# Performance work log

Hardware: AMD Instinct MI355X
Metric: run time of the kernel (lower is better)

The kernel has to match this reference:

```python
import jax, jax.numpy as jnp
import numpy as np

B, C, H, W, Q = 8, 64, 32, 32, 8
K = 2 ** Q  # codebook size = 256


def setup_inputs() -> dict:
    key = jax.random.key(0)
    k0, k1, k2, k3, k4, k5 = jax.random.split(key, 6)
    x = jax.random.normal(k0, (B, C, H, W), dtype=jnp.float32)
    # grouped 1x1 conv C -> Q*C with groups=C: per-channel weight [C, Q]
    w_pre = jax.random.normal(k1, (C, Q), dtype=jnp.float32) * 0.1
    b_pre = jax.random.normal(k2, (C, Q), dtype=jnp.float32) * 0.01
    # codebook init: uniform(-1/2^Q, 1/2^Q) as in nn.Embedding init in the module
    codebook = jax.random.uniform(k3, (K, Q), dtype=jnp.float32, minval=-1.0 / K, maxval=1.0 / K)
    # grouped 1x1 conv Q*C -> C with groups=C: per-channel weight [C, Q]
    w_after = jax.random.normal(k4, (C, Q), dtype=jnp.float32) * 0.1
    b_after = jax.random.normal(k5, (C,), dtype=jnp.float32) * 0.01
    return {"x": x, "w_pre": w_pre, "b_pre": b_pre, "codebook": codebook,
            "w_after": w_after, "b_after": b_after}


def reference(x, w_pre, b_pre, codebook, w_after, b_after):
    sg = jax.lax.stop_gradient
    Bn, Cn, Hn, Wn = x.shape
    Qn = w_pre.shape[1]
    # pre_quant: grouped 1x1 conv (groups=C): each input channel c -> Q outputs
    # y[b,c,q,h,w] = x[b,c,h,w] * w_pre[c,q] + b_pre[c,q]
    y = x[:, :, None, :, :] * w_pre[None, :, :, None, None] + b_pre[None, :, :, None, None]
    # torch permutes [B, C*Q, H, W] -> [B, H, W, C*Q] then reshapes to (-1, Q);
    # out-channel order is c*Q+q, so rows are (b,h,w,c) blocks of Q features.
    xq = jnp.transpose(y, (0, 3, 4, 1, 2))  # [B, H, W, C, Q]
    flat = xq.reshape(-1, Qn)  # [N, Q]
    cb = codebook  # [K, Q]
    # squared euclidean distances [N, K]
    dist = (jnp.sum(flat * flat, axis=1, keepdims=True)
            + jnp.sum(cb * cb, axis=1)
            - 2.0 * flat @ cb.T)
    idx = jnp.argmin(dist, axis=1)  # [N]
    out = cb[idx]  # gather == one-hot @ codebook, same math
    kl_loss = (jnp.mean((sg(out) - flat) ** 2)
               + 0.25 * jnp.mean((out - sg(flat)) ** 2))
    # straight-through
    bit = flat + sg(out - flat)  # [N, Q]
    bit5 = bit.reshape(Bn, Hn, Wn, Cn, Qn)
    bit_cqhw = jnp.transpose(bit5, (0, 3, 4, 1, 2))  # [B, C, Q, H, W]
    bit_out = bit_cqhw.reshape(Bn, Cn * Qn, Hn, Wn)
    # after_quant: grouped 1x1 conv (groups=C): Q inputs per channel -> 1 output
    recon = (jnp.einsum('bcqhw,cq->bchw', bit_cqhw, w_after)
             + b_after[None, :, None, None])
    return kl_loss, bit_out, recon
```

## Files before the change

kernel.cpp:

```cpp
#include <hip/hip_runtime.h>
#include <float.h>

#define NB 8
#define NC 64
#define NH 32
#define NW 32
#define NQ 8
#define NK 256
#define NROWS (NB*NC*NH*NW)
#define TPB 256
#define RPB 1024
#define NBLK2 (NROWS/RPB)
#define BIT_OFF 1
#define REC_OFF (1 + NROWS*NQ)

#define WS_BREAKS(ws) ((double*)(ws))
#define WS_SEGCB(ws)  ((float*)((char*)(ws) + 196608))
#define WS_SEGR(ws)   ((float*)((char*)(ws) + 720896))
#define WS_SEGBG(ws)  ((double*)((char*)(ws) + 786432))
#define WS_ALPHA(ws)  ((double*)((char*)(ws) + 1048576))
#define WS_M(ws)      ((int*)((char*)(ws) + 1049088))
#define WS_PART(ws)   ((double*)((char*)(ws) + 1049856))

__global__ __launch_bounds__(64) void vq_envelope(
    const float* __restrict__ w_pre,
    const float* __restrict__ b_pre,
    const float* __restrict__ codebook,
    const float* __restrict__ w_after,
    const float* __restrict__ b_after,
    double* __restrict__ g_breaks,
    float* __restrict__ g_segcb,
    float* __restrict__ g_segR,
    double* __restrict__ g_segBG,
    double* __restrict__ g_alpha,
    int* __restrict__ g_m)
{
    __shared__ double2 s_PS[NK];
    __shared__ int     s_win[NK];

    const int c = blockIdx.x;
    const int lane = threadIdx.x;

    double wp[NQ], bp[NQ], wa[NQ];
    double sw2 = 0.0, swb = 0.0, sb2 = 0.0;
    #pragma unroll
    for (int q = 0; q < NQ; q++) {
        wp[q] = (double)w_pre[c*NQ + q];
        bp[q] = (double)b_pre[c*NQ + q];
        wa[q] = (double)w_after[c*NQ + q];
        sw2 = fma(wp[q], wp[q], sw2);
        swb = fma(wp[q], bp[q], swb);
        sb2 = fma(bp[q], bp[q], sb2);
    }
    const double ba = (double)b_after[c];

    double P[4], S[4];
    #pragma unroll
    for (int i = 0; i < 4; i++) {
        const int k = 4*lane + i;
        double c2 = 0.0, A = 0.0, Bv = 0.0;
        #pragma unroll
        for (int q = 0; q < NQ; q++) {
            double cv = (double)codebook[k*NQ + q];
            c2 = fma(cv, cv, c2);
            A  = fma(wp[q], cv, A);
            Bv = fma(bp[q], cv, Bv);
        }
        P[i] = c2 - 2.0*Bv;
        S[i] = -2.0*A;
        s_PS[k] = make_double2(P[i], S[i]);
    }

    double bs = S[0], bP = P[0];
    int bk = 4*lane;
    #pragma unroll
    for (int i = 1; i < 4; i++) {
        const int k = 4*lane + i;
        if (S[i] > bs || (S[i] == bs && (P[i] < bP || (P[i] == bP && k < bk)))) {
            bs = S[i]; bP = P[i]; bk = k;
        }
    }
    #pragma unroll
    for (int off = 32; off; off >>= 1) {
        double os = __shfl_xor(bs, off, 64);
        double oP = __shfl_xor(bP, off, 64);
        int    ok = __shfl_xor(bk, off, 64);
        if (os > bs || (os == bs && (oP < bP || (oP == bP && ok < bk)))) {
            bs = os; bP = oP; bk = ok;
        }
    }
    int cur = bk;
    if (lane == 0) s_win[0] = cur;
    int m = 1;

    while (m < NK) {
        const double2 psi = s_PS[cur];
        const double Pi = psi.x, Si = psi.y;

        double cx = DBL_MAX, cs = 0.0;
        int cj = NK;
        #pragma unroll
        for (int i = 0; i < 4; i++) {
            const int k = 4*lane + i;
            if (S[i] < Si) {
                double t = (P[i] - Pi) / (Si - S[i]);
                if (t < cx || (t == cx && (S[i] < cs || (S[i] == cs && k < cj)))) {
                    cx = t; cs = S[i]; cj = k;
                }
            }
        }
        #pragma unroll
        for (int off = 32; off; off >>= 1) {
            double ox = __shfl_xor(cx, off, 64);
            double os = __shfl_xor(cs, off, 64);
            int    oj = __shfl_xor(cj, off, 64);
            if (ox < cx || (ox == cx && (os < cs || (os == cs && oj < cj)))) {
                cx = ox; cs = os; cj = oj;
            }
        }
        if (cx == DBL_MAX) break;
        if (lane == 0) {
            g_breaks[c*NK + m] = cx;
            s_win[m] = cj;
        }
        cur = cj;
        m++;
    }
    if (lane == 0) {
        g_m[c] = m;
        g_alpha[c] = sw2;
    }

    for (int i = lane; i < m; i += 64) {
        const int j = s_win[i];
        double c2 = 0.0, A = 0.0, Bv = 0.0, R = ba;
        #pragma unroll
        for (int q = 0; q < NQ; q++) {
            float cf = codebook[j*NQ + q];
            g_segcb[(c*NK + i)*NQ + q] = cf;
            double cv = (double)cf;
            c2 = fma(cv, cv, c2);
            A  = fma(wp[q], cv, A);
            Bv = fma(bp[q], cv, Bv);
            R  = fma(wa[q], cv, R);
        }
        g_segR[c*NK + i] = (float)R;
        g_segBG[(c*NK + i)*2 + 0] = (-2.0*A) + 2.0*swb;
        g_segBG[(c*NK + i)*2 + 1] = (c2 - 2.0*Bv) + sb2;
    }
}

__global__ __launch_bounds__(TPB) void vq_main(
    const float* __restrict__ x,
    const double* __restrict__ g_breaks,
    const float* __restrict__ g_segcb,
    const float* __restrict__ g_segR,
    const double* __restrict__ g_segBG,
    const double* __restrict__ g_alpha,
    const int* __restrict__ g_m,
    float* __restrict__ out,
    double* __restrict__ partial)
{
    __shared__ double s_brk[NK];
    __shared__ float  s_cb[NK][9];
    __shared__ float  s_R[NK];
    __shared__ double s_bg[NK][2];
    __shared__ double s_alpha;
    __shared__ double s_part[TPB/64];

    const int tid = threadIdx.x;
    const int bc = blockIdx.x;
    const int b = bc >> 6;
    const int c = bc & 63;
    const int rowbase = bc * RPB;

    const int m = g_m[c];
    if (tid == 0) s_alpha = g_alpha[c];
    if (tid < m) {
        s_brk[tid] = (tid == 0) ? -DBL_MAX : g_breaks[c*NK + tid];
        const float4* cb4 = (const float4*)(g_segcb + (c*NK + tid)*NQ);
        float4 c0 = cb4[0], c1 = cb4[1];
        s_cb[tid][0] = c0.x; s_cb[tid][1] = c0.y; s_cb[tid][2] = c0.z; s_cb[tid][3] = c0.w;
        s_cb[tid][4] = c1.x; s_cb[tid][5] = c1.y; s_cb[tid][6] = c1.z; s_cb[tid][7] = c1.w;
        s_R[tid] = g_segR[c*NK + tid];
        const double2 bg = *(const double2*)(g_segBG + (c*NK + tid)*2);
        s_bg[tid][0] = bg.x; s_bg[tid][1] = bg.y;
    }
    __syncthreads();

    const double alpha = s_alpha;
    const int bq0 = BIT_OFF + (b*512 + c*8)*1024;

    double ktot = 0.0;
    #pragma unroll
    for (int r = 0; r < 4; r++) {
        const int hw  = r*256 + tid;
        const int gid = rowbase + hw;
        const double xv = (double)x[gid];

        int lo = 0, hi = m - 1;
        while (lo < hi) {
            int mid = (lo + hi + 1) >> 1;
            if (s_brk[mid] <= xv) lo = mid; else hi = mid - 1;
        }

        #pragma unroll
        for (int q = 0; q < NQ; q++)
            out[bq0 + q*1024 + hw] = s_cb[lo][q];
        out[REC_OFF + gid] = s_R[lo];

        ktot += fma(xv, fma(xv, alpha, s_bg[lo][0]), s_bg[lo][1]);
    }

    #pragma unroll
    for (int off = 32; off; off >>= 1)
        ktot += __shfl_down(ktot, off, 64);
    if ((tid & 63) == 0) s_part[tid >> 6] = ktot;
    __syncthreads();
    if (tid == 0)
        partial[blockIdx.x] = s_part[0] + s_part[1] + s_part[2] + s_part[3];
}

__global__ __launch_bounds__(TPB) void vq_fin(
    const double* __restrict__ partial,
    float* __restrict__ out)
{
    double s = 0.0;
    for (int i = threadIdx.x; i < NBLK2; i += TPB) s += partial[i];
    #pragma unroll
    for (int off = 32; off; off >>= 1)
        s += __shfl_down(s, off, 64);
    __shared__ double sp[TPB/64];
    if ((threadIdx.x & 63) == 0) sp[threadIdx.x >> 6] = s;
    __syncthreads();
    if (threadIdx.x == 0) {
        double m = (sp[0] + sp[1] + sp[2] + sp[3]) / (double)(NROWS * NQ);
        out[0] = (float)(1.25 * m);
    }
}

extern "C" void kernel_launch(void* const* d_in, const int* in_sizes, int n_in,
                              void* d_out, int out_size, void* d_ws, size_t ws_size,
                              hipStream_t stream) {
    const float* x        = (const float*)d_in[0];
    const float* w_pre    = (const float*)d_in[1];
    const float* b_pre    = (const float*)d_in[2];
    const float* codebook = (const float*)d_in[3];
    const float* w_after  = (const float*)d_in[4];
    const float* b_after  = (const float*)d_in[5];
    float* out = (float*)d_out;

    vq_envelope<<<NC, 64, 0, stream>>>(w_pre, b_pre, codebook, w_after, b_after,
                                       WS_BREAKS(d_ws), WS_SEGCB(d_ws),
                                       WS_SEGR(d_ws), WS_SEGBG(d_ws), WS_ALPHA(d_ws),
                                       WS_M(d_ws));
    vq_main<<<NBLK2, TPB, 0, stream>>>(x, WS_BREAKS(d_ws), WS_SEGCB(d_ws),
                                       WS_SEGR(d_ws), WS_SEGBG(d_ws), WS_ALPHA(d_ws),
                                       WS_M(d_ws), out, WS_PART(d_ws));
    vq_fin<<<1, TPB, 0, stream>>>(WS_PART(d_ws), out);
}
```

Baseline: 27.54 us.

## Build lower envelope in parallel per codebook entry instead of sequential hull walk

Replaces the serial envelope walk, one wave iterating over up to 256 segments with shuffle reductions each step, with a fully parallel construction. Each of 256 threads takes one codebook line, finds its tightest lower and upper intersection bounds against all other lines to decide whether it lies on the envelope, then computes its rank by counting alive lines with smaller breakpoints. This removes the long dependent chain in the envelope kernel at the cost of O(K^2) comparisons per channel and exact-comparison tie handling that may differ subtly from the serial version.

```diff
diff --git a/kernel.cpp b/kernel.cpp
--- a/kernel.cpp
+++ b/kernel.cpp
@@ -22,7 +22,7 @@
 #define WS_M(ws)      ((int*)((char*)(ws) + 1049088))
 #define WS_PART(ws)   ((double*)((char*)(ws) + 1049856))
 
-__global__ __launch_bounds__(64) void vq_envelope(
+__global__ __launch_bounds__(NK) void vq_envelope(
     const float* __restrict__ w_pre,
     const float* __restrict__ b_pre,
     const float* __restrict__ codebook,
@@ -36,10 +36,11 @@
     int* __restrict__ g_m)
 {
     __shared__ double2 s_PS[NK];
-    __shared__ int     s_win[NK];
+    __shared__ double  s_Ln[NK], s_Ld[NK];
+    __shared__ unsigned char s_hasL[NK], s_alive[NK];
 
     const int c = blockIdx.x;
-    const int lane = threadIdx.x;
+    const int i = threadIdx.x;
 
     double wp[NQ], bp[NQ], wa[NQ];
     double sw2 = 0.0, swb = 0.0, sb2 = 0.0;
@@ -54,99 +55,83 @@
     }
     const double ba = (double)b_after[c];
 
-    double P[4], S[4];
-    #pragma unroll
-    for (int i = 0; i < 4; i++) {
-        const int k = 4*lane + i;
-        double c2 = 0.0, A = 0.0, Bv = 0.0;
+    double c2 = 0.0, A = 0.0, Bv = 0.0;
+    #pragma unroll
+    for (int q = 0; q < NQ; q++) {
+        double cv = (double)codebook[i*NQ + q];
+        c2 = fma(cv, cv, c2);
+        A  = fma(wp[q], cv, A);
+        Bv = fma(bp[q], cv, Bv);
+    }
+    const double Pi = c2 - 2.0*Bv;
+    const double Si = -2.0*A;
+    s_PS[i] = make_double2(Pi, Si);
+    __syncthreads();
+
+    double nL = 0.0, dL = 0.0, nU = 0.0, dU = 0.0;
+    bool hasL = false, hasU = false, dead = false;
+    for (int j = 0; j < NK; j++) {
+        const double2 ps = s_PS[j];
+        if (j == i) continue;
+        const double dS = ps.y - Si;
+        if (dS > 0.0) {
+            const double n = Pi - ps.x, d = dS;
+            bool take = !hasL || (n*dL > nL*d);
+            if (take) { nL = n; dL = d; hasL = true; }
+        } else if (dS < 0.0) {
+            const double n = ps.x - Pi, d = -dS;
+            bool take = !hasU || (n*dU < nU*d);
+            if (take) { nU = n; dU = d; hasU = true; }
+        } else {
+            if (ps.x < Pi || (ps.x == Pi && j < i)) dead = true;
+        }
+    }
+    bool alive = !dead;
+    if (alive && hasL && hasU) alive = (nL*dU < nU*dL);
+    const double Lv = hasL ? (nL/dL) : -DBL_MAX;
+
+    s_Ln[i] = nL; s_Ld[i] = dL;
+    s_hasL[i] = hasL ? 1 : 0;
+    s_alive[i] = alive ? 1 : 0;
+    __syncthreads();
+
+    int rank = 0, mtot = 0;
+    for (int j = 0; j < NK; j++) {
+        if (!s_alive[j]) continue;
+        mtot++;
+        if (j == i) continue;
+        bool before;
+        const bool jHas = (s_hasL[j] != 0);
+        if (!jHas)       before = true;
+        else if (!hasL)  before = false;
+        else {
+            const double a = s_Ln[j]*dL, b2 = nL*s_Ld[j];
+            if (a < b2)      before = true;
+            else if (a > b2) before = false;
+            else {
+                const double Sj = s_PS[j].y;
+                before = (Sj > Si) || (Sj == Si && j < i);
+            }
+        }
+        if (before) rank++;
+    }
+
+    if (alive) {
+        if (rank > 0) g_breaks[c*NK + rank] = Lv;
+        double R = ba;
         #pragma unroll
         for (int q = 0; q < NQ; q++) {
-            double cv = (double)codebook[k*NQ + q];
-            c2 = fma(cv, cv, c2);
-            A  = fma(wp[q], cv, A);
-            Bv = fma(bp[q], cv, Bv);
-        }
-        P[i] = c2 - 2.0*Bv;
-        S[i] = -2.0*A;
-        s_PS[k] = make_double2(P[i], S[i]);
-    }
-
-    double bs = S[0], bP = P[0];
-    int bk = 4*lane;
-    #pragma unroll
-    for (int i = 1; i < 4; i++) {
-        const int k = 4*lane + i;
-        if (S[i] > bs || (S[i] == bs && (P[i] < bP || (P[i] == bP && k < bk)))) {
-            bs = S[i]; bP = P[i]; bk = k;
-        }
-    }
-    #pragma unroll
-    for (int off = 32; off; off >>= 1) {
-        double os = __shfl_xor(bs, off, 64);
-        double oP = __shfl_xor(bP, off, 64);
-        int    ok = __shfl_xor(bk, off, 64);
-        if (os > bs || (os == bs && (oP < bP || (oP == bP && ok < bk)))) {
-            bs = os; bP = oP; bk = ok;
-        }
-    }
-    int cur = bk;
-    if (lane == 0) s_win[0] = cur;
-    int m = 1;
-
-    while (m < NK) {
-        const double2 psi = s_PS[cur];
-        const double Pi = psi.x, Si = psi.y;
-
-        double cx = DBL_MAX, cs = 0.0;
-        int cj = NK;
-        #pragma unroll
-        for (int i = 0; i < 4; i++) {
-            const int k = 4*lane + i;
-            if (S[i] < Si) {
-                double t = (P[i] - Pi) / (Si - S[i]);
-                if (t < cx || (t == cx && (S[i] < cs || (S[i] == cs && k < cj)))) {
-                    cx = t; cs = S[i]; cj = k;
-                }
-            }
-        }
-        #pragma unroll
-        for (int off = 32; off; off >>= 1) {
-            double ox = __shfl_xor(cx, off, 64);
-            double os = __shfl_xor(cs, off, 64);
-            int    oj = __shfl_xor(cj, off, 64);
-            if (ox < cx || (ox == cx && (os < cs || (os == cs && oj < cj)))) {
-                cx = ox; cs = os; cj = oj;
-            }
-        }
-        if (cx == DBL_MAX) break;
-        if (lane == 0) {
-            g_breaks[c*NK + m] = cx;
-            s_win[m] = cj;
-        }
-        cur = cj;
-        m++;
-    }
-    if (lane == 0) {
-        g_m[c] = m;
+            const float cf = codebook[i*NQ + q];
+            g_segcb[(c*NK + rank)*NQ + q] = cf;
+            R = fma(wa[q], (double)cf, R);
+        }
+        g_segR[c*NK + rank] = (float)R;
+        g_segBG[(c*NK + rank)*2 + 0] = Si + 2.0*swb;
+        g_segBG[(c*NK + rank)*2 + 1] = Pi + sb2;
+    }
+    if (i == 0) {
+        g_m[c] = mtot;
         g_alpha[c] = sw2;
-    }
-
-    for (int i = lane; i < m; i += 64) {
-        const int j = s_win[i];
-        double c2 = 0.0, A = 0.0, Bv = 0.0, R = ba;
-        #pragma unroll
-        for (int q = 0; q < NQ; q++) {
-            float cf = codebook[j*NQ + q];
-            g_segcb[(c*NK + i)*NQ + q] = cf;
-            double cv = (double)cf;
-            c2 = fma(cv, cv, c2);
-            A  = fma(wp[q], cv, A);
-            Bv = fma(bp[q], cv, Bv);
-            R  = fma(wa[q], cv, R);
-        }
-        g_segR[c*NK + i] = (float)R;
-        g_segBG[(c*NK + i)*2 + 0] = (-2.0*A) + 2.0*swb;
-        g_segBG[(c*NK + i)*2 + 1] = (c2 - 2.0*Bv) + sb2;
     }
 }
 
@@ -250,7 +235,7 @@
     const float* b_after  = (const float*)d_in[5];
     float* out = (float*)d_out;
 
-    vq_envelope<<<NC, 64, 0, stream>>>(w_pre, b_pre, codebook, w_after, b_after,
+    vq_envelope<<<NC, NK, 0, stream>>>(w_pre, b_pre, codebook, w_after, b_after,
                                        WS_BREAKS(d_ws), WS_SEGCB(d_ws),
                                        WS_SEGR(d_ws), WS_SEGBG(d_ws), WS_ALPHA(d_ws),
                                        WS_M(d_ws));
```

New measurement: 85.64 us. 211% more time.

## Split envelope walk across four wavefronts starting at fixed x split points

Applied to the files above, without the earlier changes.

The envelope kernel now runs 256 threads per channel instead of 64. Each of the four wavefronts finds the argmin codebook entry at its own start x (-1, 0.0125, 1) and walks the lower envelope only up to the next wave's start. The partial walks are then stitched together with prefix offsets. Codebook entries are staged in LDS and the segment tables are filled in parallel from cached P/S values rather than recomputed per entry. This shortens the serial breakpoint-walk critical path. The cost is more LDS, extra synchronisation, and reliance on correct tie handling at the split points.

```diff
diff --git a/kernel.cpp b/kernel.cpp
--- a/kernel.cpp
+++ b/kernel.cpp
@@ -22,7 +22,7 @@
 #define WS_M(ws)      ((int*)((char*)(ws) + 1049088))
 #define WS_PART(ws)   ((double*)((char*)(ws) + 1049856))
 
-__global__ __launch_bounds__(64) void vq_envelope(
+__global__ __launch_bounds__(256) void vq_envelope(
     const float* __restrict__ w_pre,
     const float* __restrict__ b_pre,
     const float* __restrict__ codebook,
@@ -36,10 +36,15 @@
     int* __restrict__ g_m)
 {
     __shared__ double2 s_PS[NK];
-    __shared__ int     s_win[NK];
-
-    const int c = blockIdx.x;
-    const int lane = threadIdx.x;
+    __shared__ float   s_cbf[NK][NQ];
+    __shared__ double  l_brk[4][NK];
+    __shared__ short   l_win[4][NK];
+    __shared__ int     s_p[4];
+
+    const int c    = blockIdx.x;
+    const int t    = threadIdx.x;
+    const int w    = t >> 6;
+    const int lane = t & 63;
 
     double wp[NQ], bp[NQ], wa[NQ];
     double sw2 = 0.0, swb = 0.0, sb2 = 0.0;
@@ -54,46 +59,75 @@
     }
     const double ba = (double)b_after[c];
 
-    double P[4], S[4];
-    #pragma unroll
-    for (int i = 0; i < 4; i++) {
-        const int k = 4*lane + i;
+    {
         double c2 = 0.0, A = 0.0, Bv = 0.0;
         #pragma unroll
         for (int q = 0; q < NQ; q++) {
-            double cv = (double)codebook[k*NQ + q];
+            const float cf = codebook[t*NQ + q];
+            s_cbf[t][q] = cf;
+            const double cv = (double)cf;
             c2 = fma(cv, cv, c2);
             A  = fma(wp[q], cv, A);
             Bv = fma(bp[q], cv, Bv);
         }
-        P[i] = c2 - 2.0*Bv;
-        S[i] = -2.0*A;
-        s_PS[k] = make_double2(P[i], S[i]);
-    }
-
-    double bs = S[0], bP = P[0];
-    int bk = 4*lane;
-    #pragma unroll
-    for (int i = 1; i < 4; i++) {
-        const int k = 4*lane + i;
-        if (S[i] > bs || (S[i] == bs && (P[i] < bP || (P[i] == bP && k < bk)))) {
-            bs = S[i]; bP = P[i]; bk = k;
-        }
-    }
-    #pragma unroll
-    for (int off = 32; off; off >>= 1) {
-        double os = __shfl_xor(bs, off, 64);
-        double oP = __shfl_xor(bP, off, 64);
-        int    ok = __shfl_xor(bk, off, 64);
-        if (os > bs || (os == bs && (oP < bP || (oP == bP && ok < bk)))) {
-            bs = os; bP = oP; bk = ok;
-        }
-    }
-    int cur = bk;
-    if (lane == 0) s_win[0] = cur;
-    int m = 1;
-
-    while (m < NK) {
+        s_PS[t] = make_double2(c2 - 2.0*Bv, -2.0*A);
+    }
+    __syncthreads();
+
+    double P[4], S[4];
+    #pragma unroll
+    for (int i = 0; i < 4; i++) {
+        const double2 ps = s_PS[4*lane + i];
+        P[i] = ps.x; S[i] = ps.y;
+    }
+
+    const double Ms  = (w == 1) ? -1.0 : (w == 2) ? 0.0125 : 1.0;
+    const double Mhi = (w == 0) ? -1.0 : (w == 1) ? 0.0125
+                     : (w == 2) ? 1.0  : DBL_MAX;
+
+    int cur;
+    if (w == 0) {
+        double bs = S[0], bP = P[0];
+        int bk = 4*lane;
+        #pragma unroll
+        for (int i = 1; i < 4; i++) {
+            const int k = 4*lane + i;
+            if (S[i] > bs || (S[i] == bs && (P[i] < bP || (P[i] == bP && k < bk)))) {
+                bs = S[i]; bP = P[i]; bk = k;
+            }
+        }
+        #pragma unroll
+        for (int off = 32; off; off >>= 1) {
+            double os = __shfl_xor(bs, off, 64);
+            double oP = __shfl_xor(bP, off, 64);
+            int    ok = __shfl_xor(bk, off, 64);
+            if (os > bs || (os == bs && (oP < bP || (oP == bP && ok < bk)))) {
+                bs = os; bP = oP; bk = ok;
+            }
+        }
+        cur = bk;
+    } else {
+        double bd = fma(Ms, S[0], P[0]);
+        int bk = 4*lane;
+        #pragma unroll
+        for (int i = 1; i < 4; i++) {
+            const double d = fma(Ms, S[i], P[i]);
+            const int k = 4*lane + i;
+            if (d < bd || (d == bd && k < bk)) { bd = d; bk = k; }
+        }
+        #pragma unroll
+        for (int off = 32; off; off >>= 1) {
+            double od = __shfl_xor(bd, off, 64);
+            int    ok = __shfl_xor(bk, off, 64);
+            if (od < bd || (od == bd && ok < bk)) { bd = od; bk = ok; }
+        }
+        cur = bk;
+    }
+
+    int p = 0;
+    if (w == 0) { if (lane == 0) l_win[0][0] = (short)cur; p = 1; }
+
+    while (p < NK) {
         const double2 psi = s_PS[cur];
         const double Pi = psi.x, Si = psi.y;
 
@@ -103,9 +137,9 @@
         for (int i = 0; i < 4; i++) {
             const int k = 4*lane + i;
             if (S[i] < Si) {
-                double t = (P[i] - Pi) / (Si - S[i]);
-                if (t < cx || (t == cx && (S[i] < cs || (S[i] == cs && k < cj)))) {
-                    cx = t; cs = S[i]; cj = k;
+                const double tt = (P[i] - Pi) / (Si - S[i]);
+                if (tt < cx || (tt == cx && (S[i] < cs || (S[i] == cs && k < cj)))) {
+                    cx = tt; cs = S[i]; cj = k;
                 }
             }
         }
@@ -118,35 +152,45 @@
                 cx = ox; cs = os; cj = oj;
             }
         }
-        if (cx == DBL_MAX) break;
+        if (cx >= Mhi) break;
         if (lane == 0) {
-            g_breaks[c*NK + m] = cx;
-            s_win[m] = cj;
+            l_brk[w][p] = cx;
+            l_win[w][p] = (short)cj;
         }
         cur = cj;
-        m++;
-    }
-    if (lane == 0) {
+        p++;
+    }
+    if (lane == 0) s_p[w] = p;
+    __syncthreads();
+
+    const int o1 = s_p[0];
+    const int o2 = o1 + s_p[1];
+    const int o3 = o2 + s_p[2];
+    const int m  = o3 + s_p[3];
+
+    if (t < m) {
+        int w2, s2;
+        if      (t < o1) { w2 = 0; s2 = t; }
+        else if (t < o2) { w2 = 1; s2 = t - o1; }
+        else if (t < o3) { w2 = 2; s2 = t - o2; }
+        else             { w2 = 3; s2 = t - o3; }
+        const int j = l_win[w2][s2];
+        if (t > 0) g_breaks[c*NK + t] = l_brk[w2][s2];
+        const double2 ps = s_PS[j];
+        double R = ba;
+        #pragma unroll
+        for (int q = 0; q < NQ; q++) {
+            const float cf = s_cbf[j][q];
+            g_segcb[(c*NK + t)*NQ + q] = cf;
+            R = fma(wa[q], (double)cf, R);
+        }
+        g_segR[c*NK + t] = (float)R;
+        g_segBG[(c*NK + t)*2 + 0] = ps.y + 2.0*swb;
+        g_segBG[(c*NK + t)*2 + 1] = ps.x + sb2;
+    }
+    if (t == 0) {
         g_m[c] = m;
         g_alpha[c] = sw2;
-    }
-
-    for (int i = lane; i < m; i += 64) {
-        const int j = s_win[i];
-        double c2 = 0.0, A = 0.0, Bv = 0.0, R = ba;
-        #pragma unroll
-        for (int q = 0; q < NQ; q++) {
-            float cf = codebook[j*NQ + q];
-            g_segcb[(c*NK + i)*NQ + q] = cf;
-            double cv = (double)cf;
-            c2 = fma(cv, cv, c2);
-            A  = fma(wp[q], cv, A);
-            Bv = fma(bp[q], cv, Bv);
-            R  = fma(wa[q], cv, R);
-        }
-        g_segR[c*NK + i] = (float)R;
-        g_segBG[(c*NK + i)*2 + 0] = (-2.0*A) + 2.0*swb;
-        g_segBG[(c*NK + i)*2 + 1] = (c2 - 2.0*Bv) + sb2;
     }
 }
 
@@ -250,10 +294,10 @@
     const float* b_after  = (const float*)d_in[5];
     float* out = (float*)d_out;
 
-    vq_envelope<<<NC, 64, 0, stream>>>(w_pre, b_pre, codebook, w_after, b_after,
-                                       WS_BREAKS(d_ws), WS_SEGCB(d_ws),
-                                       WS_SEGR(d_ws), WS_SEGBG(d_ws), WS_ALPHA(d_ws),
-                                       WS_M(d_ws));
+    vq_envelope<<<NC, 256, 0, stream>>>(w_pre, b_pre, codebook, w_after, b_after,
+                                        WS_BREAKS(d_ws), WS_SEGCB(d_ws),
+                                        WS_SEGR(d_ws), WS_SEGBG(d_ws), WS_ALPHA(d_ws),
+                                        WS_M(d_ws));
     vq_main<<<NBLK2, TPB, 0, stream>>>(x, WS_BREAKS(d_ws), WS_SEGCB(d_ws),
                                        WS_SEGR(d_ws), WS_SEGBG(d_ws), WS_ALPHA(d_ws),
                                        WS_M(d_ws), out, WS_PART(d_ws));
```

After: 25.84 us. -6.2%, faster.
